# Kernel optimization log

Measured on AMD Instinct MI355X. Metric: run time of the kernel, lower is better.

The kernel has to match this reference:

```python
import jax, jax.numpy as jnp
import numpy as np

DROPOUT_P = 0.1


def setup_inputs() -> dict:
    key = jax.random.key(0)
    kq, kk, kv = jax.random.split(key, 3)
    B, S, E = 16, 2048, 128
    return {
        "query": jax.random.normal(kq, (B, S, E), dtype=jnp.float32),
        "key": jax.random.normal(kk, (B, S, E), dtype=jnp.float32),
        "value": jax.random.normal(kv, (B, S, E), dtype=jnp.float32),
    }


def reference(query, key, value):
    # attn_weights = softmax(Q K^T)  -- note: NO 1/sqrt(d) scaling in the original module
    scores = jnp.einsum("bqe,bke->bqk", query, key)  # [B, S, S]
    attn = jax.nn.softmax(scores, axis=-1)
    # dropout (training mode, p=DROPOUT_P), deterministic fixed key
    dkey = jax.random.key(42)
    keep = jax.random.bernoulli(dkey, 1.0 - DROPOUT_P, attn.shape)
    attn = jnp.where(keep, attn / (1.0 - DROPOUT_P), 0.0).astype(attn.dtype)
    return jnp.einsum("bqk,bke->bqe", attn, value)
```

## Files before the change

kernel.cpp:

```cpp
#include <hip/hip_runtime.h>
#include <hip/hip_bf16.h>
#include <stdint.h>

#define S_LEN 2048
#define E_DIM 128
#define KT 32
#define KTM 64

#define ARR_BYTES   (8u * 1024 * 1024)
#define PART_FLOATS 8320
#define PART_BYTES  ((size_t)1024 * PART_FLOATS * 4)
#define TIER_B      ((size_t)3u * ARR_BYTES)
#define TIER_A      (TIER_B + PART_BYTES)

typedef __attribute__((ext_vector_type(4))) float f32x4;
typedef __attribute__((ext_vector_type(4))) short s16x4;
typedef __attribute__((ext_vector_type(8))) short bf16x8;

__device__ __forceinline__ short f2bf(float f) {
    uint32_t u = __builtin_bit_cast(uint32_t, f);
    u += 0x7FFFu + ((u >> 16) & 1u);
    return (short)(u >> 16);
}
__device__ __forceinline__ float bf2f(short h) {
    uint32_t u = ((uint32_t)(uint16_t)h) << 16;
    return __builtin_bit_cast(float, u);
}
__device__ __forceinline__ uint32_t cvtpk_bf16(float lo, float hi) {
    uint32_t d;
    asm volatile("v_cvt_pk_bf16_f32 %0, %1, %2" : "=v"(d) : "v"(lo), "v"(hi));
    return d;
}

__device__ __forceinline__ void threefry_g(uint32_t k0, uint32_t k1,
                                           uint32_t c0, uint32_t c1,
                                           uint32_t& y0, uint32_t& y1) {
    uint32_t ks2 = k0 ^ k1 ^ 0x1BD11BDAu;
    uint32_t x0 = c0 + k0, x1 = c1 + k1;
#define TF_R(rr) { x0 += x1; x1 = __builtin_amdgcn_alignbit(x1, x1, 32u - rr); x1 ^= x0; }
    TF_R(13) TF_R(15) TF_R(26) TF_R(6)
    x0 += k1;  x1 += ks2 + 1u;
    TF_R(17) TF_R(29) TF_R(16) TF_R(24)
    x0 += ks2; x1 += k0 + 2u;
    TF_R(13) TF_R(15) TF_R(26) TF_R(6)
    x0 += k0;  x1 += k1 + 3u;
    TF_R(17) TF_R(29) TF_R(16) TF_R(24)
    x0 += k1;  x1 += ks2 + 4u;
    TF_R(13) TF_R(15) TF_R(26) TF_R(6)
    x0 += ks2; x1 += k0 + 5u;
#undef TF_R
    y0 = x0; y1 = x1;
}

__device__ __forceinline__ bool keep_bit(uint32_t j) {
    uint32_t y0, y1;
    threefry_g(0u, 42u, 0u, j, y0, y1);
    return (y0 ^ y1) < 0xE6666600u;
}

__global__ __launch_bounds__(256, 4)
void convert_kv(const float* __restrict__ Kg, const float* __restrict__ Vg,
                short* __restrict__ KH, short* __restrict__ KL,
                short* __restrict__ VT) {
    __shared__ short vs[64][130];
    const int blk = blockIdx.x;
    const int b = blk >> 5, t = blk & 31;
    const size_t base = ((size_t)b * S_LEN + (size_t)t * 64) * E_DIM;
    const int e0 = (threadIdx.x & 31) * 4;
    const int rb = threadIdx.x >> 5;
    #pragma unroll
    for (int it = 0; it < 8; ++it) {
        int row = it * 8 + rb;
        f32x4 kv = *(const f32x4*)(Kg + base + row * E_DIM + e0);
        s16x4 h, lo;
        #pragma unroll
        for (int i = 0; i < 4; ++i) {
            short hh = f2bf(kv[i]);
            h[i]  = hh;
            lo[i] = f2bf(kv[i] - bf2f(hh));
        }
        *(s16x4*)(KH + base + row * E_DIM + e0) = h;
        *(s16x4*)(KL + base + row * E_DIM + e0) = lo;
        f32x4 vv = *(const f32x4*)(Vg + base + row * E_DIM + e0);
        #pragma unroll
        for (int i = 0; i < 4; ++i) vs[row][e0 + i] = f2bf(vv[i]);
    }
    __syncthreads();
    const int e = threadIdx.x >> 1;
    const int k2 = (threadIdx.x & 1) * 32;
    short* dst = VT + ((size_t)b * E_DIM + e) * S_LEN + t * 64 + k2;
    #pragma unroll
    for (int i = 0; i < 32; i += 4) {
        s16x4 v;
        #pragma unroll
        for (int q2 = 0; q2 < 4; ++q2) v[q2] = vs[k2 + i + q2][e];
        *(s16x4*)(dst + i) = v;
    }
}

template<int NSPLIT>
__global__ __launch_bounds__(256, 4)
void attn5(const float* __restrict__ Qg, const short* __restrict__ KH,
           const short* __restrict__ KL, const short* __restrict__ VT,
           float* __restrict__ outp) {
    __shared__ __attribute__((aligned(16))) short kh[KT * E_DIM];
    __shared__ __attribute__((aligned(16))) short kl[KT * E_DIM];
    __shared__ __attribute__((aligned(16))) short vt[E_DIM * 40];
    __shared__ __attribute__((aligned(16))) uint32_t plt[4][16 * 20];
    __shared__ uint32_t mldsT[(S_LEN / NSPLIT) / 32][64];

    const int tid = threadIdx.x;
    const int w   = tid >> 6;
    const int ln  = tid & 63;
    const int r   = ln & 15;
    const int g   = ln >> 4;
    const int nwg = 512 * NSPLIT;
    const int wg  = (blockIdx.x & 7) * (nwg >> 3) + (blockIdx.x >> 3);
    const int t   = wg / NSPLIT;
    const int s   = wg % NSPLIT;
    const int b   = t >> 5;
    const int q0  = (t & 31) << 6;
    const int k0g = s * (S_LEN / NSPLIT);
    const int NT  = (S_LEN / NSPLIT) / KT;
    const size_t boff = (size_t)b * S_LEN * E_DIM;

    bf16x8 qh[4], ql[4];
    #pragma unroll
    for (int ec = 0; ec < 4; ++ec) {
        const float* src = Qg + boff + (size_t)(q0 + w * 16 + r) * E_DIM + ec * 32 + g * 8;
        f32x4 va = *(const f32x4*)(src);
        f32x4 vb2 = *(const f32x4*)(src + 4);
        #pragma unroll
        for (int i = 0; i < 4; ++i) {
            short hh = f2bf(va[i]);
            qh[ec][i] = hh;
            ql[ec][i] = f2bf(va[i] - bf2f(hh));
            short h2 = f2bf(vb2[i]);
            qh[ec][4 + i] = h2;
            ql[ec][4 + i] = f2bf(vb2[i] - bf2f(h2));
        }
    }

    {
        const int segs = (S_LEN / NSPLIT) / 64;
        const uint32_t jb = (((uint32_t)b << 11) + (uint32_t)q0) * 2048u
                          + (uint32_t)k0g + (uint32_t)ln;
        for (int i = 0; i < 16 * segs; ++i) {
            int rr  = w * 16 + i / segs;
            int seg = i % segs;
            uint32_t j = jb + (uint32_t)rr * 2048u + (uint32_t)(seg * 64);
            uint64_t m = __ballot(keep_bit(j));
            if (ln < 2) mldsT[seg * 2 + ln][rr] = (uint32_t)(m >> (ln * 32));
        }
    }

    const short* KHb = KH + ((size_t)b * S_LEN + k0g) * E_DIM;
    const short* KLb = KL + ((size_t)b * S_LEN + k0g) * E_DIM;
    const short* VTb = VT + (size_t)b * E_DIM * S_LEN + k0g;

    bf16x8 skh[2], skl[2], sv0, sv1;
    const int se0 = (tid & 15) * 8;
    const int srl = tid >> 4;
    const int sve = tid >> 1;
    const int svh = tid & 1;
#define LOAD_TILE(ktt)                                                          \
    {                                                                           \
        _Pragma("unroll")                                                       \
        for (int p = 0; p < 2; ++p) {                                           \
            int row = srl + p * 16;                                             \
            skh[p] = *(const bf16x8*)(KHb + (size_t)((ktt) * KT + row) * E_DIM + se0); \
            skl[p] = *(const bf16x8*)(KLb + (size_t)((ktt) * KT + row) * E_DIM + se0); \
        }                                                                       \
        const short* vsrc = VTb + (size_t)sve * S_LEN + (ktt) * KT + svh * 16;  \
        sv0 = *(const bf16x8*)(vsrc);                                           \
        sv1 = *(const bf16x8*)(vsrc + 8);                                       \
    }
    LOAD_TILE(0)

    f32x4 oacc[8];
    #pragma unroll
    for (int i = 0; i < 8; ++i) oacc[i] = f32x4{0.f, 0.f, 0.f, 0.f};
    float mrun = -1e30f, den = 0.f;

    for (int kt = 0; kt < NT; ++kt) {
        __syncthreads();
        {
            #pragma unroll
            for (int p = 0; p < 2; ++p) {
                int row = srl + p * 16;
                int idx = (row * E_DIM + se0) ^ ((row & 7) << 3);
                *(bf16x8*)(kh + idx) = skh[p];
                *(bf16x8*)(kl + idx) = skl[p];
            }
            const int swv = ((sve >> 3) & 1) << 1;
            *(bf16x8*)(vt + sve * 40 + (((svh * 2) ^ swv) << 3))     = sv0;
            *(bf16x8*)(vt + sve * 40 + (((svh * 2 + 1) ^ swv) << 3)) = sv1;
        }
        __syncthreads();

        f32x4 sc[2];
        #pragma unroll
        for (int c = 0; c < 2; ++c) {
            f32x4 acc = f32x4{0.f, 0.f, 0.f, 0.f};
            int krow = c * 16 + r;
            int sw = (krow & 7) << 3;
            #pragma unroll
            for (int ec = 0; ec < 4; ++ec) {
                int idx = (krow * E_DIM + ec * 32 + g * 8) ^ sw;
                bf16x8 bh = *(const bf16x8*)(kh + idx);
                bf16x8 bl = *(const bf16x8*)(kl + idx);
                acc = __builtin_amdgcn_mfma_f32_16x16x32_bf16(bh, qh[ec], acc, 0, 0, 0);
                acc = __builtin_amdgcn_mfma_f32_16x16x32_bf16(bl, qh[ec], acc, 0, 0, 0);
                acc = __builtin_amdgcn_mfma_f32_16x16x32_bf16(bh, ql[ec], acc, 0, 0, 0);
            }
            sc[c] = acc;
        }

        float pmax = fmaxf(fmaxf(fmaxf(sc[0][0], sc[0][1]), fmaxf(sc[0][2], sc[0][3])),
                           fmaxf(fmaxf(sc[1][0], sc[1][1]), fmaxf(sc[1][2], sc[1][3])));
        pmax = fmaxf(pmax, __shfl_xor(pmax, 16));
        pmax = fmaxf(pmax, __shfl_xor(pmax, 32));
        if (__any(pmax - mrun > 8.0f)) {
            float mnew = fmaxf(mrun, pmax);
            float scl = __expf(mrun - mnew);
            mrun = mnew;
            den *= scl;
            #pragma unroll
            for (int et = 0; et < 8; ++et) oacc[et] *= scl;
        }
        float rs = 0.f;
        #pragma unroll
        for (int c = 0; c < 2; ++c) {
            #pragma unroll
            for (int reg = 0; reg < 4; ++reg) {
                float p = __expf(sc[c][reg] - mrun);
                sc[c][reg] = p;
                rs += p;
            }
        }
        rs += __shfl_xor(rs, 16);
        rs += __shfl_xor(rs, 32);
        den += rs;

        if (kt + 1 < NT) LOAD_TILE(kt + 1)

        uint32_t bits = mldsT[kt][w * 16 + r] >> (g * 4);
        float pm[2][4];
        #pragma unroll
        for (int c = 0; c < 2; ++c) {
            #pragma unroll
            for (int reg = 0; reg < 4; ++reg)
                pm[c][reg] = ((bits >> (c * 16 + reg)) & 1u)
                               ? sc[c][reg] * (1.0f / 0.9f) : 0.0f;
        }
        uint2 pk0 = { cvtpk_bf16(pm[0][0], pm[0][1]), cvtpk_bf16(pm[0][2], pm[0][3]) };
        uint2 pk1 = { cvtpk_bf16(pm[1][0], pm[1][1]), cvtpk_bf16(pm[1][2], pm[1][3]) };
        *(uint2*)(&plt[w][r * 20 + g * 2])     = pk0;
        *(uint2*)(&plt[w][r * 20 + 8 + g * 2]) = pk1;
        bf16x8 pfrag = *(const bf16x8*)((const short*)&plt[w][0] + r * 40 + g * 8);

        const int swr = ((r >> 3) & 1) << 1;
        #pragma unroll
        for (int et = 0; et < 8; ++et) {
            const short* vp = vt + (et * 16 + r) * 40 + ((g ^ swr) << 3);
            bf16x8 av = *(const bf16x8*)vp;
            oacc[et] = __builtin_amdgcn_mfma_f32_16x16x32_bf16(av, pfrag, oacc[et], 0, 0, 0);
        }
    }

    const int q = w * 16 + r;
    if (NSPLIT == 1) {
        float inv = 1.0f / den;
        float* dst = outp + boff + (size_t)(q0 + q) * E_DIM;
        #pragma unroll
        for (int et = 0; et < 8; ++et) {
            f32x4 o = oacc[et] * inv;
            *(f32x4*)(dst + et * 16 + g * 4) = o;
        }
    } else {
        float* pb = outp + (size_t)wg * PART_FLOATS;
        if (g == 0) {
            pb[q]      = mrun;
            pb[64 + q] = den;
        }
        #pragma unroll
        for (int et = 0; et < 8; ++et)
            *(f32x4*)(pb + 128 + q * E_DIM + et * 16 + g * 4) = oacc[et];
    }
}

__global__ __launch_bounds__(256, 8)
void merge_k(const float* __restrict__ part, float* __restrict__ Og) {
    const int t = blockIdx.x;
    const int b = t >> 5;
    const int q0 = (t & 31) << 6;
    const float* p0 = part + (size_t)(t * 2 + 0) * PART_FLOATS;
    const float* p1 = part + (size_t)(t * 2 + 1) * PART_FLOATS;
    float* dst = Og + (size_t)b * S_LEN * E_DIM + (size_t)q0 * E_DIM;
    for (int i = 0; i < 32; ++i) {
        int idx = i * 256 + threadIdx.x;
        int row = idx >> 7, e = idx & 127;
        float m0 = p0[row], m1 = p1[row];
        float mm = fmaxf(m0, m1);
        float s0 = __expf(m0 - mm), s1 = __expf(m1 - mm);
        float d = p0[64 + row] * s0 + p1[64 + row] * s1;
        float o = p0[128 + row * E_DIM + e] * s0 + p1[128 + row * E_DIM + e] * s1;
        dst[row * E_DIM + e] = o / d;
    }
}

__global__ __launch_bounds__(256, 2)
void attn_mono(const float* __restrict__ Qg, const float* __restrict__ Kg,
               const float* __restrict__ Vg, float* __restrict__ Og) {
    __shared__ short kh[KTM * E_DIM];
    __shared__ short kl[KTM * E_DIM];
    __shared__ short vt[E_DIM * 66];
    __shared__ short pl[4][16 * 64];

    const int tid = threadIdx.x;
    const int w   = tid >> 6;
    const int ln  = tid & 63;
    const int r   = ln & 15;
    const int g   = ln >> 4;
    const int bid = blockIdx.x;
    const int b   = bid >> 5;
    const int q0  = (bid & 31) << 6;
    const size_t boff = (size_t)b * S_LEN * E_DIM;

    {
        const float* src = Qg + boff + (size_t)q0 * E_DIM;
        const int e0 = (tid & 31) * 4;
        const int rb = tid >> 5;
        #pragma unroll
        for (int it = 0; it < 8; ++it) {
            int row = it * 8 + rb;
            f32x4 v = *(const f32x4*)(src + row * E_DIM + e0);
            s16x4 h, lo;
            #pragma unroll
            for (int i = 0; i < 4; ++i) {
                short hh = f2bf(v[i]);
                h[i]  = hh;
                lo[i] = f2bf(v[i] - bf2f(hh));
            }
            int idx = (row * E_DIM + e0) ^ ((row & 7) << 3);
            *(s16x4*)(kh + idx) = h;
            *(s16x4*)(kl + idx) = lo;
        }
    }
    __syncthreads();
    bf16x8 qh[4], ql[4];
    {
        int row = w * 16 + r;
        #pragma unroll
        for (int ec = 0; ec < 4; ++ec) {
            int idx = (row * E_DIM + ec * 32 + g * 8) ^ ((row & 7) << 3);
            qh[ec] = *(const bf16x8*)(kh + idx);
            ql[ec] = *(const bf16x8*)(kl + idx);
        }
    }
    f32x4 oacc[8];
    #pragma unroll
    for (int i = 0; i < 8; ++i) oacc[i] = f32x4{0.f, 0.f, 0.f, 0.f};
    float mrun[4] = {-1e30f, -1e30f, -1e30f, -1e30f};
    float den[4]  = {0.f, 0.f, 0.f, 0.f};

    for (int kt = 0; kt < S_LEN / KTM; ++kt) {
        __syncthreads();
        {
            const float* src = Kg + boff + (size_t)(kt * KTM) * E_DIM;
            const int e0 = (tid & 31) * 4;
            const int rb = tid >> 5;
            #pragma unroll
            for (int it = 0; it < 8; ++it) {
                int row = it * 8 + rb;
                f32x4 v = *(const f32x4*)(src + row * E_DIM + e0);
                s16x4 h, lo;
                #pragma unroll
                for (int i = 0; i < 4; ++i) {
                    short hh = f2bf(v[i]);
                    h[i]  = hh;
                    lo[i] = f2bf(v[i] - bf2f(hh));
                }
                int idx = (row * E_DIM + e0) ^ ((row & 7) << 3);
                *(s16x4*)(kh + idx) = h;
                *(s16x4*)(kl + idx) = lo;
            }
        }
        {
            const float* src = Vg + boff + (size_t)(kt * KTM) * E_DIM;
            const int e0 = (tid & 31) * 4;
            const int kb = (tid >> 5) * 2;
            #pragma unroll
            for (int it = 0; it < 4; ++it) {
                int k = it * 16 + kb;
                f32x4 a  = *(const f32x4*)(src + k * E_DIM + e0);
                f32x4 c2 = *(const f32x4*)(src + (k + 1) * E_DIM + e0);
                #pragma unroll
                for (int ci = 0; ci < 4; ++ci) {
                    uint32_t pack = (uint32_t)(uint16_t)f2bf(a[ci]) |
                                    ((uint32_t)(uint16_t)f2bf(c2[ci]) << 16);
                    *(uint32_t*)(vt + (e0 + ci) * 66 + k) = pack;
                }
            }
        }
        __syncthreads();
        f32x4 sc[4];
        #pragma unroll
        for (int c = 0; c < 4; ++c) {
            f32x4 acc = f32x4{0.f, 0.f, 0.f, 0.f};
            int krow = c * 16 + r;
            int sw = (krow & 7) << 3;
            #pragma unroll
            for (int ec = 0; ec < 4; ++ec) {
                int idx = (krow * E_DIM + ec * 32 + g * 8) ^ sw;
                bf16x8 bh = *(const bf16x8*)(kh + idx);
                bf16x8 bl = *(const bf16x8*)(kl + idx);
                acc = __builtin_amdgcn_mfma_f32_16x16x32_bf16(qh[ec], bh, acc, 0, 0, 0);
                acc = __builtin_amdgcn_mfma_f32_16x16x32_bf16(ql[ec], bh, acc, 0, 0, 0);
                acc = __builtin_amdgcn_mfma_f32_16x16x32_bf16(qh[ec], bl, acc, 0, 0, 0);
            }
            sc[c] = acc;
        }
        float scale[4];
        #pragma unroll
        for (int reg = 0; reg < 4; ++reg) {
            float v0 = fmaxf(fmaxf(sc[0][reg], sc[1][reg]),
                             fmaxf(sc[2][reg], sc[3][reg]));
            v0 = fmaxf(v0, __shfl_xor(v0, 1));
            v0 = fmaxf(v0, __shfl_xor(v0, 2));
            v0 = fmaxf(v0, __shfl_xor(v0, 4));
            v0 = fmaxf(v0, __shfl_xor(v0, 8));
            float mnew = fmaxf(mrun[reg], v0);
            scale[reg] = __expf(mrun[reg] - mnew);
            mrun[reg] = mnew;
        }
        float rs[4] = {0.f, 0.f, 0.f, 0.f};
        #pragma unroll
        for (int c = 0; c < 4; ++c) {
            #pragma unroll
            for (int reg = 0; reg < 4; ++reg) {
                float p = __expf(sc[c][reg] - mrun[reg]);
                sc[c][reg] = p;
                rs[reg] += p;
            }
        }
        #pragma unroll
        for (int reg = 0; reg < 4; ++reg) {
            float v0 = rs[reg];
            v0 += __shfl_xor(v0, 1);
            v0 += __shfl_xor(v0, 2);
            v0 += __shfl_xor(v0, 4);
            v0 += __shfl_xor(v0, 8);
            den[reg] = den[reg] * scale[reg] + v0;
        }
        #pragma unroll
        for (int et = 0; et < 8; ++et) {
            #pragma unroll
            for (int reg = 0; reg < 4; ++reg) oacc[et][reg] *= scale[reg];
        }
        #pragma unroll
        for (int c = 0; c < 4; ++c) {
            int kcol = kt * KTM + c * 16 + r;
            #pragma unroll
            for (int reg = 0; reg < 4; ++reg) {
                int row = g * 4 + reg;
                uint32_t q = (uint32_t)(q0 + w * 16 + row);
                uint32_t j = (((uint32_t)b << 11) + q) * 2048u + (uint32_t)kcol;
                float pm = keep_bit(j) ? sc[c][reg] * (1.0f / 0.9f) : 0.0f;
                int idx = (row * 64 + (c * 16 + r)) ^ ((row & 7) << 3);
                pl[w][idx] = f2bf(pm);
            }
        }
        bf16x8 pa[2];
        #pragma unroll
        for (int st = 0; st < 2; ++st) {
            int idx = (r * 64 + st * 32 + g * 8) ^ ((r & 7) << 3);
            pa[st] = *(const bf16x8*)(&pl[w][0] + idx);
        }
        #pragma unroll
        for (int et = 0; et < 8; ++et) {
            int e = et * 16 + r;
            f32x4 o = oacc[et];
            #pragma unroll
            for (int st = 0; st < 2; ++st) {
                union { bf16x8 v; uint32_t u[4]; } vb;
                #pragma unroll
                for (int i2 = 0; i2 < 4; ++i2)
                    vb.u[i2] = *(const uint32_t*)(vt + e * 66 + st * 32 + g * 8 + i2 * 2);
                o = __builtin_amdgcn_mfma_f32_16x16x32_bf16(pa[st], vb.v, o, 0, 0, 0);
            }
            oacc[et] = o;
        }
    }
    float inv[4];
    #pragma unroll
    for (int reg = 0; reg < 4; ++reg) inv[reg] = 1.0f / den[reg];
    float* dst = Og + boff + (size_t)q0 * E_DIM;
    #pragma unroll
    for (int et = 0; et < 8; ++et) {
        #pragma unroll
        for (int reg = 0; reg < 4; ++reg) {
            int row = w * 16 + g * 4 + reg;
            int e = et * 16 + r;
            dst[row * E_DIM + e] = oacc[et][reg] * inv[reg];
        }
    }
}

extern "C" void kernel_launch(void* const* d_in, const int* in_sizes, int n_in,
                              void* d_out, int out_size, void* d_ws, size_t ws_size,
                              hipStream_t stream) {
    (void)in_sizes; (void)n_in; (void)out_size;
    const float* Q = (const float*)d_in[0];
    const float* K = (const float*)d_in[1];
    const float* V = (const float*)d_in[2];
    float* O = (float*)d_out;
    if (ws_size >= TIER_B) {
        short* KH = (short*)d_ws;
        short* KL = (short*)((char*)d_ws + ARR_BYTES);
        short* VT = (short*)((char*)d_ws + 2u * ARR_BYTES);
        hipLaunchKernelGGL(convert_kv, dim3(512), dim3(256), 0, stream, K, V, KH, KL, VT);
        if (ws_size >= TIER_A) {
            float* part = (float*)((char*)d_ws + TIER_B);
            hipLaunchKernelGGL((attn5<2>), dim3(1024), dim3(256), 0, stream,
                               Q, KH, KL, VT, part);
            hipLaunchKernelGGL(merge_k, dim3(512), dim3(256), 0, stream, part, O);
        } else {
            hipLaunchKernelGGL((attn5<1>), dim3(512), dim3(256), 0, stream,
                               Q, KH, KL, VT, O);
        }
    } else {
        hipLaunchKernelGGL(attn_mono, dim3(512), dim3(256), 0, stream, Q, K, V, O);
    }
}
```

Baseline: 249.3 us.

## Use 512-thread blocks with 128-query tiles and 4-way key split

The attention kernel now runs 8 waves per block covering 128 query rows, so each staged K/V tile in shared memory is reused by twice as many queries. The key dimension is split four ways instead of two, and the merge kernel is generalized to combine NSPLIT partials. This roughly halves K/V global and shared-memory staging traffic per query. In exchange it costs more shared memory and registers per block, which may lower occupancy, and it writes and merges more partial results.

```diff
diff --git a/kernel.cpp b/kernel.cpp
--- a/kernel.cpp
+++ b/kernel.cpp
@@ -7,11 +7,11 @@
 #define KT 32
 #define KTM 64
 
-#define ARR_BYTES   (8u * 1024 * 1024)
-#define PART_FLOATS 8320
-#define PART_BYTES  ((size_t)1024 * PART_FLOATS * 4)
-#define TIER_B      ((size_t)3u * ARR_BYTES)
-#define TIER_A      (TIER_B + PART_BYTES)
+#define ARR_BYTES    (8u * 1024 * 1024)
+#define PART2_FLOATS 16640
+#define TIER_B       ((size_t)3u * ARR_BYTES)
+#define TIER_A2      (TIER_B + (size_t)512 * PART2_FLOATS * 4)
+#define TIER_A4      (TIER_B + (size_t)1024 * PART2_FLOATS * 4)
 
 typedef __attribute__((ext_vector_type(4))) float f32x4;
 typedef __attribute__((ext_vector_type(4))) short s16x4;
@@ -99,29 +99,29 @@
 }
 
 template<int NSPLIT>
-__global__ __launch_bounds__(256, 4)
-void attn5(const float* __restrict__ Qg, const short* __restrict__ KH,
+__global__ __launch_bounds__(512, 4)
+void attn9(const float* __restrict__ Qg, const short* __restrict__ KH,
            const short* __restrict__ KL, const short* __restrict__ VT,
            float* __restrict__ outp) {
+    constexpr int NT = (S_LEN / NSPLIT) / KT;
     __shared__ __attribute__((aligned(16))) short kh[KT * E_DIM];
     __shared__ __attribute__((aligned(16))) short kl[KT * E_DIM];
     __shared__ __attribute__((aligned(16))) short vt[E_DIM * 40];
-    __shared__ __attribute__((aligned(16))) uint32_t plt[4][16 * 20];
-    __shared__ uint32_t mldsT[(S_LEN / NSPLIT) / 32][64];
+    __shared__ __attribute__((aligned(16))) uint32_t plt[8][16 * 20];
+    __shared__ uint32_t mldsT[NT][128];
 
     const int tid = threadIdx.x;
     const int w   = tid >> 6;
     const int ln  = tid & 63;
     const int r   = ln & 15;
     const int g   = ln >> 4;
-    const int nwg = 512 * NSPLIT;
+    const int nwg = 256 * NSPLIT;
     const int wg  = (blockIdx.x & 7) * (nwg >> 3) + (blockIdx.x >> 3);
     const int t   = wg / NSPLIT;
     const int s   = wg % NSPLIT;
-    const int b   = t >> 5;
-    const int q0  = (t & 31) << 6;
+    const int b   = t >> 4;
+    const int q0  = (t & 15) << 7;
     const int k0g = s * (S_LEN / NSPLIT);
-    const int NT  = (S_LEN / NSPLIT) / KT;
     const size_t boff = (size_t)b * S_LEN * E_DIM;
 
     bf16x8 qh[4], ql[4];
@@ -158,22 +158,16 @@
     const short* KLb = KL + ((size_t)b * S_LEN + k0g) * E_DIM;
     const short* VTb = VT + (size_t)b * E_DIM * S_LEN + k0g;
 
-    bf16x8 skh[2], skl[2], sv0, sv1;
+    bf16x8 skh, skl, svv;
     const int se0 = (tid & 15) * 8;
     const int srl = tid >> 4;
-    const int sve = tid >> 1;
-    const int svh = tid & 1;
+    const int sve = tid >> 2;
+    const int svq = tid & 3;
 #define LOAD_TILE(ktt)                                                          \
     {                                                                           \
-        _Pragma("unroll")                                                       \
-        for (int p = 0; p < 2; ++p) {                                           \
-            int row = srl + p * 16;                                             \
-            skh[p] = *(const bf16x8*)(KHb + (size_t)((ktt) * KT + row) * E_DIM + se0); \
-            skl[p] = *(const bf16x8*)(KLb + (size_t)((ktt) * KT + row) * E_DIM + se0); \
-        }                                                                       \
-        const short* vsrc = VTb + (size_t)sve * S_LEN + (ktt) * KT + svh * 16;  \
-        sv0 = *(const bf16x8*)(vsrc);                                           \
-        sv1 = *(const bf16x8*)(vsrc + 8);                                       \
+        skh = *(const bf16x8*)(KHb + (size_t)((ktt) * KT + srl) * E_DIM + se0); \
+        skl = *(const bf16x8*)(KLb + (size_t)((ktt) * KT + srl) * E_DIM + se0); \
+        svv = *(const bf16x8*)(VTb + (size_t)sve * S_LEN + (ktt) * KT + svq * 8); \
     }
     LOAD_TILE(0)
 
@@ -185,16 +179,11 @@
     for (int kt = 0; kt < NT; ++kt) {
         __syncthreads();
         {
-            #pragma unroll
-            for (int p = 0; p < 2; ++p) {
-                int row = srl + p * 16;
-                int idx = (row * E_DIM + se0) ^ ((row & 7) << 3);
-                *(bf16x8*)(kh + idx) = skh[p];
-                *(bf16x8*)(kl + idx) = skl[p];
-            }
+            int idx = (srl * E_DIM + se0) ^ ((srl & 7) << 3);
+            *(bf16x8*)(kh + idx) = skh;
+            *(bf16x8*)(kl + idx) = skl;
             const int swv = ((sve >> 3) & 1) << 1;
-            *(bf16x8*)(vt + sve * 40 + (((svh * 2) ^ swv) << 3))     = sv0;
-            *(bf16x8*)(vt + sve * 40 + (((svh * 2 + 1) ^ swv) << 3)) = sv1;
+            *(bf16x8*)(vt + sve * 40 + ((svq ^ swv) << 3)) = svv;
         }
         __syncthreads();
 
@@ -278,33 +267,41 @@
             *(f32x4*)(dst + et * 16 + g * 4) = o;
         }
     } else {
-        float* pb = outp + (size_t)wg * PART_FLOATS;
+        float* pb = outp + (size_t)wg * PART2_FLOATS;
         if (g == 0) {
-            pb[q]      = mrun;
-            pb[64 + q] = den;
+            pb[q]       = mrun;
+            pb[128 + q] = den;
         }
         #pragma unroll
         for (int et = 0; et < 8; ++et)
-            *(f32x4*)(pb + 128 + q * E_DIM + et * 16 + g * 4) = oacc[et];
-    }
-}
-
+            *(f32x4*)(pb + 256 + q * E_DIM + et * 16 + g * 4) = oacc[et];
+    }
+}
+
+template<int NSPLIT>
 __global__ __launch_bounds__(256, 8)
-void merge_k(const float* __restrict__ part, float* __restrict__ Og) {
+void merge9(const float* __restrict__ part, float* __restrict__ Og) {
     const int t = blockIdx.x;
-    const int b = t >> 5;
-    const int q0 = (t & 31) << 6;
-    const float* p0 = part + (size_t)(t * 2 + 0) * PART_FLOATS;
-    const float* p1 = part + (size_t)(t * 2 + 1) * PART_FLOATS;
+    const int b = t >> 4;
+    const int q0 = (t & 15) << 7;
+    const float* ps[NSPLIT];
+    #pragma unroll
+    for (int s = 0; s < NSPLIT; ++s)
+        ps[s] = part + (size_t)(t * NSPLIT + s) * PART2_FLOATS;
     float* dst = Og + (size_t)b * S_LEN * E_DIM + (size_t)q0 * E_DIM;
-    for (int i = 0; i < 32; ++i) {
+    for (int i = 0; i < 64; ++i) {
         int idx = i * 256 + threadIdx.x;
         int row = idx >> 7, e = idx & 127;
-        float m0 = p0[row], m1 = p1[row];
-        float mm = fmaxf(m0, m1);
-        float s0 = __expf(m0 - mm), s1 = __expf(m1 - mm);
-        float d = p0[64 + row] * s0 + p1[64 + row] * s1;
-        float o = p0[128 + row * E_DIM + e] * s0 + p1[128 + row * E_DIM + e] * s1;
+        float mm = ps[0][row];
+        #pragma unroll
+        for (int s = 1; s < NSPLIT; ++s) mm = fmaxf(mm, ps[s][row]);
+        float d = 0.f, o = 0.f;
+        #pragma unroll
+        for (int s = 0; s < NSPLIT; ++s) {
+            float sc = __expf(ps[s][row] - mm);
+            d += ps[s][128 + row] * sc;
+            o += ps[s][256 + row * E_DIM + e] * sc;
+        }
         dst[row * E_DIM + e] = o / d;
     }
 }
@@ -520,13 +517,18 @@
         short* KL = (short*)((char*)d_ws + ARR_BYTES);
         short* VT = (short*)((char*)d_ws + 2u * ARR_BYTES);
         hipLaunchKernelGGL(convert_kv, dim3(512), dim3(256), 0, stream, K, V, KH, KL, VT);
-        if (ws_size >= TIER_A) {
+        if (ws_size >= TIER_A4) {
             float* part = (float*)((char*)d_ws + TIER_B);
-            hipLaunchKernelGGL((attn5<2>), dim3(1024), dim3(256), 0, stream,
+            hipLaunchKernelGGL((attn9<4>), dim3(1024), dim3(512), 0, stream,
                                Q, KH, KL, VT, part);
-            hipLaunchKernelGGL(merge_k, dim3(512), dim3(256), 0, stream, part, O);
+            hipLaunchKernelGGL((merge9<4>), dim3(256), dim3(256), 0, stream, part, O);
+        } else if (ws_size >= TIER_A2) {
+            float* part = (float*)((char*)d_ws + TIER_B);
+            hipLaunchKernelGGL((attn9<2>), dim3(512), dim3(512), 0, stream,
+                               Q, KH, KL, VT, part);
+            hipLaunchKernelGGL((merge9<2>), dim3(256), dim3(256), 0, stream, part, O);
         } else {
-            hipLaunchKernelGGL((attn5<1>), dim3(512), dim3(256), 0, stream,
+            hipLaunchKernelGGL((attn9<1>), dim3(256), dim3(512), 0, stream,
                                Q, KH, KL, VT, O);
         }
     } else {
```

New measurement: 221.7 us (median of 2 runs). 1.12x faster.
